# Kernel optimization log

Measured on AMD Instinct MI355X. Metric: run time of the kernel, lower is better.

The kernel has to match this reference:

```python
import jax, jax.numpy as jnp
import numpy as np

H = 4          # num attention heads
C1 = 64        # channel_num[0]
C2 = 128       # channel_num[1]
KV = C1 + C2   # 192
MLP = C1 * 4   # expand_ratio=4


def _layernorm(x, g, b, eps=1e-6):
    m = jnp.mean(x, axis=-1, keepdims=True)
    v = jnp.mean((x - m) ** 2, axis=-1, keepdims=True)
    return (x - m) * jax.lax.rsqrt(v + eps) * g + b


def setup_inputs() -> dict:
    key = jax.random.key(0)
    ks = jax.random.split(key, 12)
    B, N = 8, 3136
    s_q = 1.0 / np.sqrt(C1)
    s_kv = 1.0 / np.sqrt(KV)
    return {
        "emb1": jax.random.normal(ks[0], (B, N, C1), jnp.float32),
        "emb2": jax.random.normal(ks[1], (B, N, C2), jnp.float32),
        # per-head projection weights (nn.Linear convention: y = x @ W.T)
        "Wq": jax.random.uniform(ks[2], (H, C1, C1), jnp.float32, -s_q, s_q),
        "Wk": jax.random.uniform(ks[3], (H, KV, KV), jnp.float32, -s_kv, s_kv),
        "Wv": jax.random.uniform(ks[4], (H, KV, KV), jnp.float32, -s_kv, s_kv),
        "Wout": jax.random.uniform(ks[5], (C1, C1), jnp.float32, -s_q, s_q),
        "ln1_g": jnp.ones((C1,), jnp.float32),
        "ln1_b": jnp.zeros((C1,), jnp.float32),
        "lnall_g": jnp.ones((KV,), jnp.float32),
        "lnall_b": jnp.zeros((KV,), jnp.float32),
        "ffn_g": jnp.ones((C1,), jnp.float32),
        "ffn_b": jnp.zeros((C1,), jnp.float32),
        "fc1_w": jax.random.uniform(ks[6], (MLP, C1), jnp.float32, -s_q, s_q),
        "fc1_b": jnp.zeros((MLP,), jnp.float32),
        "fc2_w": jax.random.uniform(ks[7], (C1, MLP), jnp.float32, -1.0 / np.sqrt(MLP), 1.0 / np.sqrt(MLP)),
        "fc2_b": jnp.zeros((C1,), jnp.float32),
    }


def reference(emb1, emb2, Wq, Wk, Wv, Wout, ln1_g, ln1_b, lnall_g, lnall_b,
              ffn_g, ffn_b, fc1_w, fc1_b, fc2_w, fc2_b):
    # emb1: [B,N,C1], emb2: [B,N,C2]
    emb_all = jnp.concatenate([emb1, emb2], axis=2)          # [B,N,KV]
    cx1 = _layernorm(emb1, ln1_g, ln1_b)                     # [B,N,C1]
    ea = _layernorm(emb_all, lnall_g, lnall_b)               # [B,N,KV]

    # batched per-head projections (replaces Python loop over ModuleList)
    qT = jnp.einsum('bnc,hdc->bhdn', cx1, Wq)                # [B,H,C1,N]
    k = jnp.einsum('bnk,hdk->bhnd', ea, Wk)                  # [B,H,N,KV]
    vT = jnp.einsum('bnk,hdk->bhdn', ea, Wv)                 # [B,H,KV,N]

    scores = jnp.einsum('bhcn,bhnk->bhck', qT, k) / np.sqrt(KV)  # [B,H,C1,KV]
    # InstanceNorm2d over spatial dims (C1, KV) per (batch, head), affine=False
    m = jnp.mean(scores, axis=(2, 3), keepdims=True)
    v = jnp.mean((scores - m) ** 2, axis=(2, 3), keepdims=True)
    scores = (scores - m) * jax.lax.rsqrt(v + 1e-5)
    probs = jax.nn.softmax(scores, axis=3)                   # softmax over KV

    ctx = jnp.einsum('bhck,bhkn->bhcn', probs, vT)           # [B,H,C1,N]
    ctx = jnp.mean(ctx, axis=1).transpose(0, 2, 1)           # mean over heads -> [B,N,C1]
    o = ctx @ Wout.T                                         # [B,N,C1]

    cx = emb1 + o                                            # residual
    x = _layernorm(cx, ffn_g, ffn_b)
    x = jax.nn.gelu(x @ fc1_w.T + fc1_b, approximate=False)
    x = x @ fc2_w.T + fc2_b
    return x + cx
```

## Files before the change

### kernel.cpp

```cpp
#include <hip/hip_runtime.h>
#include <hip/hip_bf16.h>

typedef __hip_bfloat16 bf;
typedef unsigned short ushort_t;
typedef __attribute__((ext_vector_type(8))) short short8;
typedef __attribute__((ext_vector_type(4))) float f32x4;

#define NB 8
#define SEQ 3136
#define HD 4

__device__ __forceinline__ float lo_bf(unsigned u){ return __uint_as_float(u << 16); }
__device__ __forceinline__ float hi_bf(unsigned u){ return __uint_as_float(u & 0xffff0000u); }
__device__ __forceinline__ float b16f(ushort_t s){ return __uint_as_float(((unsigned)s) << 16); }
__device__ __forceinline__ unsigned short f2bfbits(float f){
  unsigned u = __float_as_uint(f);
  unsigned r = u + 0x7fffu + ((u >> 16) & 1u);
  return (unsigned short)(r >> 16);
}
__device__ __forceinline__ float ldin(const void* p, long i, bool isbf){
  return isbf ? __bfloat162float(((const bf*)p)[i]) : ((const float*)p)[i];
}
__device__ __forceinline__ float4 ld4(const void* p, long i, bool isbf){
  if (isbf){
    uint2 u = *reinterpret_cast<const uint2*>((const unsigned short*)p + i);
    return make_float4(lo_bf(u.x), hi_bf(u.x), lo_bf(u.y), hi_bf(u.y));
  }
  const float* f = (const float*)p + i;
  return make_float4(f[0], f[1], f[2], f[3]);
}
__device__ __forceinline__ short8 ldfrag(const void* p, long i, bool isbf){
  if (isbf) return *reinterpret_cast<const short8*>((const unsigned short*)p + i);
  const float* f = (const float*)p + i;
  short8 r;
  #pragma unroll
  for (int q=0;q<8;++q) r[q] = (short)f2bfbits(f[q]);
  return r;
}
#define DTYPE_FLAG(p) (((const unsigned*)(p))[0] == 0x3F803F80u)

__device__ __forceinline__ float wsum(float v){
  #pragma unroll
  for (int o = 32; o > 0; o >>= 1) v += __shfl_xor(v, o, 64);
  return v;
}
__device__ __forceinline__ float wmax(float v){
  #pragma unroll
  for (int o = 32; o > 0; o >>= 1) v = fmaxf(v, __shfl_xor(v, o, 64));
  return v;
}

__global__ __launch_bounds__(256) void k_g(
    const void* __restrict__ emb1, const void* __restrict__ emb2,
    const void* __restrict__ g1, const void* __restrict__ b1,
    const void* __restrict__ ga, const void* __restrict__ ba,
    ushort_t* __restrict__ part, ushort_t* __restrict__ eag){
  bool isbf = DTYPE_FLAG(g1);
  __shared__ __align__(16) ushort_t z1t[64*72];
  __shared__ __align__(16) ushort_t zat[192*72];
  int tid = threadIdx.x, wave = tid >> 6, lane = tid & 63;
  int quad = lane >> 4, nl = lane & 15;
  int b = blockIdx.y, ch = blockIdx.x;
  long t0 = (long)b*SEQ + ch*64;
  float g1l = ldin(g1,lane,isbf), b1l = ldin(b1,lane,isbf);
  float ga0 = ldin(ga,lane,isbf),     ba0 = ldin(ba,lane,isbf);
  float ga1 = ldin(ga,64+lane,isbf),  ba1 = ldin(ba,64+lane,isbf);
  float ga2 = ldin(ga,128+lane,isbf), ba2 = ldin(ba,128+lane,isbf);
  #pragma unroll 4
  for (int k = 0; k < 16; ++k){
    int tok = wave*16 + k;
    long t = t0 + tok;
    float e1  = ldin(emb1, t*64 + lane, isbf);
    float e2a = ldin(emb2, t*128 + lane, isbf);
    float e2b = ldin(emb2, t*128 + 64 + lane, isbf);
    float s1 = wsum(e1), ss1 = wsum(e1*e1);
    float m1 = s1*(1.f/64.f);
    float r1 = rsqrtf(fmaxf(ss1*(1.f/64.f) - m1*m1, 0.f) + 1e-6f);
    z1t[lane*72 + tok] = f2bfbits((e1 - m1)*r1*g1l + b1l);
    float s23 = wsum(e2a+e2b), ss23 = wsum(e2a*e2a + e2b*e2b);
    float ma = (s1+s23)*(1.f/192.f);
    float ra = rsqrtf(fmaxf((ss1+ss23)*(1.f/192.f) - ma*ma, 0.f) + 1e-6f);
    unsigned short za0 = f2bfbits((e1  - ma)*ra*ga0 + ba0);
    unsigned short za1 = f2bfbits((e2a - ma)*ra*ga1 + ba1);
    unsigned short za2 = f2bfbits((e2b - ma)*ra*ga2 + ba2);
    zat[lane*72 + tok]       = za0;
    zat[(64+lane)*72 + tok]  = za1;
    zat[(128+lane)*72 + tok] = za2;
    eag[t*192 + lane]       = za0;
    eag[t*192 + 64 + lane]  = za1;
    eag[t*192 + 128 + lane] = za2;
  }
  __syncthreads();
  short8 a0 = *reinterpret_cast<const short8*>(&z1t[(wave*16+nl)*72 + quad*8]);
  short8 a1 = *reinterpret_cast<const short8*>(&z1t[(wave*16+nl)*72 + 32 + quad*8]);
  ushort_t* P = part + ((long)b*49 + ch)*12288;
  #pragma unroll
  for (int nt = 0; nt < 12; ++nt){
    f32x4 cd = {0.f,0.f,0.f,0.f};
    short8 b0 = *reinterpret_cast<const short8*>(&zat[(nt*16+nl)*72 + quad*8]);
    cd = __builtin_amdgcn_mfma_f32_16x16x32_bf16(a0, b0, cd, 0, 0, 0);
    short8 b1v = *reinterpret_cast<const short8*>(&zat[(nt*16+nl)*72 + 32 + quad*8]);
    cd = __builtin_amdgcn_mfma_f32_16x16x32_bf16(a1, b1v, cd, 0, 0, 0);
    #pragma unroll
    for (int reg = 0; reg < 4; ++reg)
      P[(wave*16 + quad*4 + reg)*192 + nt*16 + nl] = f2bfbits(cd[reg]);
  }
}

__global__ __launch_bounds__(64) void k_red(
    const ushort_t* __restrict__ part, float* __restrict__ G){
  int idx4 = blockIdx.x*64 + threadIdx.x;
  int b = idx4 / 3072, e4 = idx4 - b*3072;
  const ushort_t* p = part + (long)b*49*12288 + e4*4;
  float s0=0.f, s1=0.f, s2=0.f, s3=0.f;
  #pragma unroll
  for (int ch = 0; ch < 49; ++ch){
    uint2 u = *reinterpret_cast<const uint2*>(p + (long)ch*12288);
    s0 += lo_bf(u.x); s1 += hi_bf(u.x); s2 += lo_bf(u.y); s3 += hi_bf(u.y);
  }
  ((float4*)G)[idx4] = make_float4(s0,s1,s2,s3);
}

__global__ __launch_bounds__(256) void k_s(
    const float* __restrict__ G, const void* __restrict__ Wq, const void* __restrict__ Wk,
    const void* __restrict__ lng, float* __restrict__ S){
  bool isbf = DTYPE_FLAG(lng);
  __shared__ __align__(16) ushort_t sGb[64*200];
  __shared__ __align__(16) ushort_t sT[48*72];
  int ec = blockIdx.x, h = blockIdx.y, b = blockIdx.z;
  int e0 = ec*48;
  int tid = threadIdx.x, wave = tid >> 6, lane = tid & 63;
  int quad = lane >> 4, nl = lane & 15;
  const float4* Gb4 = (const float4*)(G + (long)b*12288);
  for (int i16 = tid; i16 < 3072; i16 += 256){
    float4 v = Gb4[i16];
    int e = i16*4; int c = e/192, j = e - c*192;
    unsigned lo = (unsigned)f2bfbits(v.x) | ((unsigned)f2bfbits(v.y) << 16);
    unsigned hi = (unsigned)f2bfbits(v.z) | ((unsigned)f2bfbits(v.w) << 16);
    *reinterpret_cast<uint2*>(&sGb[c*200 + j]) = make_uint2(lo, hi);
  }
  __syncthreads();
  long wk0 = (long)h*36864;
  short8 aG[6];
  #pragma unroll
  for (int ks = 0; ks < 6; ++ks)
    aG[ks] = *reinterpret_cast<const short8*>(&sGb[(wave*16+nl)*200 + ks*32 + quad*8]);
  #pragma unroll
  for (int nt = 0; nt < 3; ++nt){
    f32x4 cd = {0.f,0.f,0.f,0.f};
    #pragma unroll
    for (int ks = 0; ks < 6; ++ks){
      short8 bw = ldfrag(Wk, wk0 + (long)(e0 + nt*16+nl)*192 + ks*32 + quad*8, isbf);
      cd = __builtin_amdgcn_mfma_f32_16x16x32_bf16(aG[ks], bw, cd, 0, 0, 0);
    }
    #pragma unroll
    for (int reg = 0; reg < 4; ++reg)
      sT[(nt*16+nl)*72 + wave*16 + quad*4 + reg] = f2bfbits(cd[reg]);
  }
  __syncthreads();
  long wq0 = (long)h*4096;
  short8 aQ[2];
  #pragma unroll
  for (int ks = 0; ks < 2; ++ks)
    aQ[ks] = ldfrag(Wq, wq0 + (long)(wave*16+nl)*64 + ks*32 + quad*8, isbf);
  const float scale = 0.07216878364870323f;
  float* Sb = S + ((long)b*HD + h)*12288;
  #pragma unroll
  for (int nt = 0; nt < 3; ++nt){
    f32x4 cd = {0.f,0.f,0.f,0.f};
    #pragma unroll
    for (int ks = 0; ks < 2; ++ks){
      short8 bt = *reinterpret_cast<const short8*>(&sT[(nt*16+nl)*72 + ks*32 + quad*8]);
      cd = __builtin_amdgcn_mfma_f32_16x16x32_bf16(aQ[ks], bt, cd, 0, 0, 0);
    }
    #pragma unroll
    for (int reg = 0; reg < 4; ++reg)
      Sb[(wave*16 + quad*4 + reg)*192 + e0 + nt*16 + nl] = cd[reg]*scale;
  }
}

__global__ __launch_bounds__(256) void k_smpv(
    const float* __restrict__ S, const void* __restrict__ Wv,
    const void* __restrict__ lng, float* __restrict__ Mh){
  bool isbf = DTYPE_FLAG(lng);
  __shared__ __align__(16) float sP[64*196];
  __shared__ __align__(16) unsigned sWv[192*52];
  __shared__ float red[8];
  __shared__ float stat[2];
  int jc = blockIdx.x, h = blockIdx.y, b = blockIdx.z;
  const float* Sb = S + ((long)b*HD + h)*12288;
  int tid = threadIdx.x, wave = tid >> 6, lane = tid & 63;
  long wv0 = (long)h*36864;
  float ps = 0.f, pss = 0.f;
  const float4* Sb4 = (const float4*)Sb;
  for (int i16 = tid; i16 < 3072; i16 += 256){
    float4 v = Sb4[i16];
    int e = i16*4; int c = e/192, j = e - c*192;
    *reinterpret_cast<float4*>(&sP[c*196 + j]) = v;
    ps += v.x + v.y + v.z + v.w;
    pss += v.x*v.x + v.y*v.y + v.z*v.z + v.w*v.w;
  }
  if (isbf){
    const unsigned short* wvp = (const unsigned short*)Wv + wv0 + jc*96;
    for (int idx = tid; idx < 4608; idx += 256){
      int r = idx/24, c2 = idx - r*24;
      uint2 v = *reinterpret_cast<const uint2*>(wvp + (long)r*192 + c2*4);
      *reinterpret_cast<uint2*>(&sWv[r*52 + c2*2]) = v;
    }
  } else {
    for (int idx = tid; idx < 9216; idx += 256){
      int r = idx/48, c = idx - r*48;
      float a0 = ldin(Wv, wv0 + (long)r*192 + jc*96 + c*2,     false);
      float a1 = ldin(Wv, wv0 + (long)r*192 + jc*96 + c*2 + 1, false);
      sWv[r*52 + c] = (unsigned)f2bfbits(a0) | ((unsigned)f2bfbits(a1) << 16);
    }
  }
  ps = wsum(ps); pss = wsum(pss);
  if (lane == 0){ red[wave] = ps; red[4+wave] = pss; }
  __syncthreads();
  if (tid == 0){
    float s  = red[0]+red[1]+red[2]+red[3];
    float s2 = red[4]+red[5]+red[6]+red[7];
    float m = s * (1.f/12288.f);
    stat[0] = m;
    stat[1] = rsqrtf(fmaxf(s2*(1.f/12288.f) - m*m, 0.f) + 1e-5f);
  }
  __syncthreads();
  float m = stat[0], r = stat[1];
  for (int rr = 0; rr < 16; ++rr){
    int row = wave*16 + rr;
    float v0 = (sP[row*196+lane]     - m)*r;
    float v1 = (sP[row*196+64+lane]  - m)*r;
    float v2 = (sP[row*196+128+lane] - m)*r;
    float mx = wmax(fmaxf(v0, fmaxf(v1, v2)));
    float e0 = __expf(v0-mx), e1 = __expf(v1-mx), e2 = __expf(v2-mx);
    float inv = 1.f / wsum(e0+e1+e2);
    sP[row*196+lane]     = e0*inv;
    sP[row*196+64+lane]  = e1*inv;
    sP[row*196+128+lane] = e2*inv;
  }
  __syncthreads();
  int ty = tid >> 4, tx = tid & 15;
  int j0 = jc*96 + tx*6;
  float acc[4][6];
  #pragma unroll
  for (int i=0;i<4;++i) for (int q=0;q<6;++q) acc[i][q]=0.f;
  #pragma unroll 2
  for (int e = 0; e < 192; ++e){
    float p4[4];
    #pragma unroll
    for (int i=0;i<4;++i) p4[i] = sP[(ty*4+i)*196 + e];
    unsigned wa = sWv[e*52 + tx*3];
    unsigned wb = sWv[e*52 + tx*3 + 1];
    unsigned wc = sWv[e*52 + tx*3 + 2];
    float w0 = lo_bf(wa), w1 = hi_bf(wa), w2 = lo_bf(wb),
          w3 = hi_bf(wb), w4 = lo_bf(wc), w5 = hi_bf(wc);
    #pragma unroll
    for (int i=0;i<4;++i){
      acc[i][0] = fmaf(p4[i], w0, acc[i][0]);
      acc[i][1] = fmaf(p4[i], w1, acc[i][1]);
      acc[i][2] = fmaf(p4[i], w2, acc[i][2]);
      acc[i][3] = fmaf(p4[i], w3, acc[i][3]);
      acc[i][4] = fmaf(p4[i], w4, acc[i][4]);
      acc[i][5] = fmaf(p4[i], w5, acc[i][5]);
    }
  }
  float* Mb = Mh + ((long)b*HD + h)*12288;
  #pragma unroll
  for (int i=0;i<4;++i)
    #pragma unroll
    for (int q=0;q<6;++q)
      Mb[(ty*4+i)*192 + j0 + q] = acc[i][q];
}

__global__ __launch_bounds__(256) void k_w2(
    const float* __restrict__ Mh, const void* __restrict__ Wout,
    const void* __restrict__ lng, ushort_t* __restrict__ W2){
  bool isbf = DTYPE_FLAG(lng);
  __shared__ __align__(16) float sM[64*49];
  int jc = blockIdx.x, b = blockIdx.y;
  int tid = threadIdx.x;
  for (int idx = tid; idx < 3072; idx += 256){
    int c = idx/48, j = idx - c*48;
    long base = (long)b*HD*12288 + c*192 + jc*48 + j;
    float s = Mh[base] + Mh[base+12288] + Mh[base+2*12288] + Mh[base+3*12288];
    sM[c*49 + j] = 0.25f*s;
  }
  __syncthreads();
  int ty = tid >> 4, tx = tid & 15;
  float acc[4][3];
  #pragma unroll
  for (int i=0;i<4;++i) for (int q=0;q<3;++q) acc[i][q]=0.f;
  for (int c = 0; c < 64; c += 4){
    float4 w4[4];
    #pragma unroll
    for (int i=0;i<4;++i) w4[i] = ld4(Wout, (long)(ty*4+i)*64 + c, isbf);
    float ww[4][4];
    #pragma unroll
    for (int i=0;i<4;++i){ ww[i][0]=w4[i].x; ww[i][1]=w4[i].y; ww[i][2]=w4[i].z; ww[i][3]=w4[i].w; }
    #pragma unroll
    for (int u = 0; u < 4; ++u){
      float t3[3];
      #pragma unroll
      for (int q=0;q<3;++q) t3[q] = sM[(c+u)*49 + tx*3 + q];
      #pragma unroll
      for (int i=0;i<4;++i)
        #pragma unroll
        for (int q=0;q<3;++q) acc[i][q] = fmaf(ww[i][u], t3[q], acc[i][q]);
    }
  }
  ushort_t* W2b = W2 + (long)b*12288;
  #pragma unroll
  for (int i=0;i<4;++i)
    #pragma unroll
    for (int q=0;q<3;++q)
      W2b[(ty*4+i)*192 + jc*48 + tx*3 + q] = f2bfbits(acc[i][q]);
}

__global__ __launch_bounds__(256) void k_tail(
    const void* __restrict__ emb1, const ushort_t* __restrict__ eag,
    const ushort_t* __restrict__ W2g,
    const void* __restrict__ ffg, const void* __restrict__ ffb,
    const void* __restrict__ f1w, const void* __restrict__ f1b,
    const void* __restrict__ f2w, const void* __restrict__ f2b,
    const void* __restrict__ lng, void* __restrict__ out){
  bool isbf = DTYPE_FLAG(lng);
  __shared__ __align__(16) ushort_t sCX[16*72];
  __shared__ __align__(16) ushort_t sX[16*88];
  __shared__ __align__(16) ushort_t sH[16*280];
  int tid = threadIdx.x, wave = tid >> 6, lane = tid & 63;
  int quad = lane >> 4, nl = lane & 15;
  int b = blockIdx.y;
  long tbase = (long)b*SEQ + blockIdx.x*16;

  short8 aO[6];
  #pragma unroll
  for (int kt = 0; kt < 6; ++kt)
    aO[kt] = *reinterpret_cast<const short8*>(eag + (tbase + nl)*192 + kt*32 + quad*8);
  const ushort_t* W2b = W2g + (long)b*12288;
  {
    f32x4 cd = {0.f,0.f,0.f,0.f};
    #pragma unroll
    for (int kt = 0; kt < 6; ++kt){
      short8 bf8 = *reinterpret_cast<const short8*>(W2b + (wave*16+nl)*192 + kt*32 + quad*8);
      cd = __builtin_amdgcn_mfma_f32_16x16x32_bf16(aO[kt], bf8, cd, 0, 0, 0);
    }
    #pragma unroll
    for (int reg = 0; reg < 4; ++reg){
      int tokl = quad*4 + reg;
      int chn = wave*16 + nl;
      float e1v = ldin(emb1, (tbase + tokl)*64 + chn, isbf);
      sCX[tokl*72 + chn] = f2bfbits(cd[reg] + e1v);
    }
  }
  __syncthreads();

  float gl = ldin(ffg, lane, isbf), bl = ldin(ffb, lane, isbf);
  #pragma unroll
  for (int k = 0; k < 4; ++k){
    int tokl = wave*4 + k;
    float c = b16f(sCX[tokl*72 + lane]);
    float s = wsum(c), ss = wsum(c*c);
    float m = s*(1.f/64.f);
    float r = rsqrtf(fmaxf(ss*(1.f/64.f) - m*m, 0.f) + 1e-6f);
    sX[tokl*88 + lane] = f2bfbits((c - m)*r*gl + bl);
  }
  __syncthreads();

  short8 aX[2];
  #pragma unroll
  for (int kt = 0; kt < 2; ++kt)
    aX[kt] = *reinterpret_cast<const short8*>(&sX[nl*88 + kt*32 + quad*8]);
  #pragma unroll
  for (int nn = 0; nn < 4; ++nn){
    int nt = wave*4 + nn;
    f32x4 cd = {0.f,0.f,0.f,0.f};
    #pragma unroll
    for (int kt = 0; kt < 2; ++kt){
      short8 bf8 = ldfrag(f1w, (long)(nt*16+nl)*64 + kt*32 + quad*8, isbf);
      cd = __builtin_amdgcn_mfma_f32_16x16x32_bf16(aX[kt], bf8, cd, 0, 0, 0);
    }
    float bb = ldin(f1b, nt*16+nl, isbf);
    #pragma unroll
    for (int reg = 0; reg < 4; ++reg){
      float v = cd[reg] + bb;
      float h = 0.5f*v*(1.f + erff(v*0.70710678118654752f));
      sH[(quad*4 + reg)*280 + nt*16 + nl] = f2bfbits(h);
    }
  }
  __syncthreads();

  short8 aH[8];
  #pragma unroll
  for (int kt = 0; kt < 8; ++kt)
    aH[kt] = *reinterpret_cast<const short8*>(&sH[nl*280 + kt*32 + quad*8]);
  {
    f32x4 cd = {0.f,0.f,0.f,0.f};
    #pragma unroll
    for (int kt = 0; kt < 8; ++kt){
      short8 bf8 = ldfrag(f2w, (long)(wave*16+nl)*256 + kt*32 + quad*8, isbf);
      cd = __builtin_amdgcn_mfma_f32_16x16x32_bf16(aH[kt], bf8, cd, 0, 0, 0);
    }
    float bb2 = ldin(f2b, wave*16+nl, isbf);
    #pragma unroll
    for (int reg = 0; reg < 4; ++reg){
      int tokl = quad*4 + reg;
      int chn = wave*16 + nl;
      float y = cd[reg] + bb2 + b16f(sCX[tokl*72 + chn]);
      if (isbf) sCX[tokl*72 + chn] = f2bfbits(y);
      else ((float*)out)[(tbase + tokl)*64 + chn] = y;
    }
  }
  if (isbf){
    __syncthreads();
    int tokl = wave*4 + (lane >> 4), prt = lane & 15;
    uint2 v = *reinterpret_cast<const uint2*>(&sCX[tokl*72 + prt*4]);
    *reinterpret_cast<uint2*>((ushort_t*)out + (tbase + tokl)*64 + prt*4) = v;
  }
}

extern "C" void kernel_launch(void* const* d_in, const int* in_sizes, int n_in,
                              void* d_out, int out_size, void* d_ws, size_t ws_size,
                              hipStream_t stream){
  const void* emb1 = d_in[0];
  const void* emb2 = d_in[1];
  const void* Wq   = d_in[2];
  const void* Wk   = d_in[3];
  const void* Wv   = d_in[4];
  const void* Wout = d_in[5];
  const void* ln1g = d_in[6];
  const void* ln1b = d_in[7];
  const void* lag  = d_in[8];
  const void* lab  = d_in[9];
  const void* ffg  = d_in[10];
  const void* ffb  = d_in[11];
  const void* f1w  = d_in[12];
  const void* f1b  = d_in[13];
  const void* f2w  = d_in[14];
  const void* f2b  = d_in[15];

  char* base = (char*)d_ws;
  ushort_t* part = (ushort_t*)base;
  ushort_t* ea   = (ushort_t*)(base + 9633792);
  float*    G    = (float*)(base + 19267584);
  float*    S    = (float*)(base + 19660800);
  float*    Mh   = (float*)(base + 21233664);
  ushort_t* W2   = (ushort_t*)(base + 22806528);

  k_g   <<<dim3(49,NB),   256, 0, stream>>>(emb1, emb2, ln1g, ln1b, lag, lab, part, ea);
  k_red <<<384,            64, 0, stream>>>(part, G);
  k_s   <<<dim3(4,HD,NB), 256, 0, stream>>>(G, Wq, Wk, ln1g, S);
  k_smpv<<<dim3(2,HD,NB), 256, 0, stream>>>(S, Wv, ln1g, Mh);
  k_w2  <<<dim3(4,NB),    256, 0, stream>>>(Mh, Wout, ln1g, W2);
  k_tail<<<dim3(196,NB),  256, 0, stream>>>(emb1, ea, W2, ffg, ffb,
                                            f1w, f1b, f2w, f2b, ln1g, d_out);
}
```

Before: 204.5 us.

## Batch loads in LayerNorm/Gram kernel and split softmax-V kernel into more blocks

k_g now issues loads for four tokens before doing their reductions, so more global-memory requests are in flight at once. k_smpv is split into four column chunks of 48 instead of two of 96, which doubles the grid from 64 to 128 blocks and stores Wv in shared memory as 16-bit values. Each block repeats the instance-norm and softmax work, so that part is now done twice as often. A tanh-based gelu helper is added but is not called by any code shown.

```diff
diff --git a/kernel.cpp b/kernel.cpp
--- a/kernel.cpp
+++ b/kernel.cpp
@@ -48,6 +48,10 @@
   #pragma unroll
   for (int o = 32; o > 0; o >>= 1) v = fmaxf(v, __shfl_xor(v, o, 64));
   return v;
+}
+__device__ __forceinline__ float gelu_f(float v){
+  float u = v*(0.7978845608f + 0.0356774081f*v*v);
+  return v * __builtin_amdgcn_rcpf(1.f + __expf(-2.f*u));
 }
 
 __global__ __launch_bounds__(256) void k_g(
@@ -66,29 +70,37 @@
   float ga0 = ldin(ga,lane,isbf),     ba0 = ldin(ba,lane,isbf);
   float ga1 = ldin(ga,64+lane,isbf),  ba1 = ldin(ba,64+lane,isbf);
   float ga2 = ldin(ga,128+lane,isbf), ba2 = ldin(ba,128+lane,isbf);
-  #pragma unroll 4
-  for (int k = 0; k < 16; ++k){
-    int tok = wave*16 + k;
-    long t = t0 + tok;
-    float e1  = ldin(emb1, t*64 + lane, isbf);
-    float e2a = ldin(emb2, t*128 + lane, isbf);
-    float e2b = ldin(emb2, t*128 + 64 + lane, isbf);
-    float s1 = wsum(e1), ss1 = wsum(e1*e1);
-    float m1 = s1*(1.f/64.f);
-    float r1 = rsqrtf(fmaxf(ss1*(1.f/64.f) - m1*m1, 0.f) + 1e-6f);
-    z1t[lane*72 + tok] = f2bfbits((e1 - m1)*r1*g1l + b1l);
-    float s23 = wsum(e2a+e2b), ss23 = wsum(e2a*e2a + e2b*e2b);
-    float ma = (s1+s23)*(1.f/192.f);
-    float ra = rsqrtf(fmaxf((ss1+ss23)*(1.f/192.f) - ma*ma, 0.f) + 1e-6f);
-    unsigned short za0 = f2bfbits((e1  - ma)*ra*ga0 + ba0);
-    unsigned short za1 = f2bfbits((e2a - ma)*ra*ga1 + ba1);
-    unsigned short za2 = f2bfbits((e2b - ma)*ra*ga2 + ba2);
-    zat[lane*72 + tok]       = za0;
-    zat[(64+lane)*72 + tok]  = za1;
-    zat[(128+lane)*72 + tok] = za2;
-    eag[t*192 + lane]       = za0;
-    eag[t*192 + 64 + lane]  = za1;
-    eag[t*192 + 128 + lane] = za2;
+  #pragma unroll
+  for (int k4 = 0; k4 < 4; ++k4){
+    float e1[4], e2a[4], e2b[4];
+    #pragma unroll
+    for (int u = 0; u < 4; ++u){
+      long t = t0 + wave*16 + k4 + u*4;
+      e1[u]  = ldin(emb1, t*64 + lane, isbf);
+      e2a[u] = ldin(emb2, t*128 + lane, isbf);
+      e2b[u] = ldin(emb2, t*128 + 64 + lane, isbf);
+    }
+    #pragma unroll
+    for (int u = 0; u < 4; ++u){
+      int tok = wave*16 + k4 + u*4;
+      long t = t0 + tok;
+      float s1 = wsum(e1[u]), ss1 = wsum(e1[u]*e1[u]);
+      float m1 = s1*(1.f/64.f);
+      float r1 = rsqrtf(fmaxf(ss1*(1.f/64.f) - m1*m1, 0.f) + 1e-6f);
+      z1t[lane*72 + tok] = f2bfbits((e1[u] - m1)*r1*g1l + b1l);
+      float s23 = wsum(e2a[u]+e2b[u]), ss23 = wsum(e2a[u]*e2a[u] + e2b[u]*e2b[u]);
+      float ma = (s1+s23)*(1.f/192.f);
+      float ra = rsqrtf(fmaxf((ss1+ss23)*(1.f/192.f) - ma*ma, 0.f) + 1e-6f);
+      unsigned short za0 = f2bfbits((e1[u]  - ma)*ra*ga0 + ba0);
+      unsigned short za1 = f2bfbits((e2a[u] - ma)*ra*ga1 + ba1);
+      unsigned short za2 = f2bfbits((e2b[u] - ma)*ra*ga2 + ba2);
+      zat[lane*72 + tok]       = za0;
+      zat[(64+lane)*72 + tok]  = za1;
+      zat[(128+lane)*72 + tok] = za2;
+      eag[t*192 + lane]       = za0;
+      eag[t*192 + 64 + lane]  = za1;
+      eag[t*192 + 128 + lane] = za2;
+    }
   }
   __syncthreads();
   short8 a0 = *reinterpret_cast<const short8*>(&z1t[(wave*16+nl)*72 + quad*8]);
@@ -184,7 +196,7 @@
     const void* __restrict__ lng, float* __restrict__ Mh){
   bool isbf = DTYPE_FLAG(lng);
   __shared__ __align__(16) float sP[64*196];
-  __shared__ __align__(16) unsigned sWv[192*52];
+  __shared__ __align__(16) ushort_t sWv[192*52];
   __shared__ float red[8];
   __shared__ float stat[2];
   int jc = blockIdx.x, h = blockIdx.y, b = blockIdx.z;
@@ -201,18 +213,16 @@
     pss += v.x*v.x + v.y*v.y + v.z*v.z + v.w*v.w;
   }
   if (isbf){
-    const unsigned short* wvp = (const unsigned short*)Wv + wv0 + jc*96;
-    for (int idx = tid; idx < 4608; idx += 256){
-      int r = idx/24, c2 = idx - r*24;
+    const ushort_t* wvp = (const ushort_t*)Wv + wv0 + jc*48;
+    for (int idx = tid; idx < 2304; idx += 256){
+      int r = idx/12, c2 = idx - r*12;
       uint2 v = *reinterpret_cast<const uint2*>(wvp + (long)r*192 + c2*4);
-      *reinterpret_cast<uint2*>(&sWv[r*52 + c2*2]) = v;
+      *reinterpret_cast<uint2*>(&sWv[r*52 + c2*4]) = v;
     }
   } else {
     for (int idx = tid; idx < 9216; idx += 256){
       int r = idx/48, c = idx - r*48;
-      float a0 = ldin(Wv, wv0 + (long)r*192 + jc*96 + c*2,     false);
-      float a1 = ldin(Wv, wv0 + (long)r*192 + jc*96 + c*2 + 1, false);
-      sWv[r*52 + c] = (unsigned)f2bfbits(a0) | ((unsigned)f2bfbits(a1) << 16);
+      sWv[r*52 + c] = f2bfbits(ldin(Wv, wv0 + (long)r*192 + jc*48 + c, false));
     }
   }
   ps = wsum(ps); pss = wsum(pss);
@@ -241,35 +251,30 @@
   }
   __syncthreads();
   int ty = tid >> 4, tx = tid & 15;
-  int j0 = jc*96 + tx*6;
-  float acc[4][6];
-  #pragma unroll
-  for (int i=0;i<4;++i) for (int q=0;q<6;++q) acc[i][q]=0.f;
-  #pragma unroll 2
+  int j0 = jc*48 + tx*3;
+  float acc[4][3];
+  #pragma unroll
+  for (int i=0;i<4;++i) for (int q=0;q<3;++q) acc[i][q]=0.f;
+  #pragma unroll 4
   for (int e = 0; e < 192; ++e){
     float p4[4];
     #pragma unroll
     for (int i=0;i<4;++i) p4[i] = sP[(ty*4+i)*196 + e];
-    unsigned wa = sWv[e*52 + tx*3];
-    unsigned wb = sWv[e*52 + tx*3 + 1];
-    unsigned wc = sWv[e*52 + tx*3 + 2];
-    float w0 = lo_bf(wa), w1 = hi_bf(wa), w2 = lo_bf(wb),
-          w3 = hi_bf(wb), w4 = lo_bf(wc), w5 = hi_bf(wc);
+    float w0 = b16f(sWv[e*52 + tx*3]);
+    float w1 = b16f(sWv[e*52 + tx*3 + 1]);
+    float w2 = b16f(sWv[e*52 + tx*3 + 2]);
     #pragma unroll
     for (int i=0;i<4;++i){
       acc[i][0] = fmaf(p4[i], w0, acc[i][0]);
       acc[i][1] = fmaf(p4[i], w1, acc[i][1]);
       acc[i][2] = fmaf(p4[i], w2, acc[i][2]);
-      acc[i][3] = fmaf(p4[i], w3, acc[i][3]);
-      acc[i][4] = fmaf(p4[i], w4, acc[i][4]);
-      acc[i][5] = fmaf(p4[i], w5, acc[i][5]);
     }
   }
   float* Mb = Mh + ((long)b*HD + h)*12288;
   #pragma unroll
   for (int i=0;i<4;++i)
     #pragma unroll
-    for (int q=0;q<6;++q)
+    for (int q=0;q<3;++q)
       Mb[(ty*4+i)*192 + j0 + q] = acc[i][q];
 }
 
@@ -450,7 +455,7 @@
   k_g   <<<dim3(49,NB),   256, 0, stream>>>(emb1, emb2, ln1g, ln1b, lag, lab, part, ea);
   k_red <<<384,            64, 0, stream>>>(part, G);
   k_s   <<<dim3(4,HD,NB), 256, 0, stream>>>(G, Wq, Wk, ln1g, S);
-  k_smpv<<<dim3(2,HD,NB), 256, 0, stream>>>(S, Wv, ln1g, Mh);
+  k_smpv<<<dim3(4,HD,NB), 256, 0, stream>>>(S, Wv, ln1g, Mh);
   k_w2  <<<dim3(4,NB),    256, 0, stream>>>(Mh, Wout, ln1g, W2);
   k_tail<<<dim3(196,NB),  256, 0, stream>>>(emb1, ea, W2, ffg, ffb,
                                             f1w, f1b, f2w, f2b, ln1g, d_out);
```

Result: slower. 217.6 us (+6.4%).

## Move instance-norm stats into k_s and split k_smpv across more blocks

Applied to the files above, without the earlier changes.

k_s now reduces per-block partial sums and sums of squares of the scores and writes them to a small stat buffer. k_smpv reads those partials instead of scanning the whole score matrix itself. That lets k_smpv split rows into 4 chunks and columns into 4 chunks, giving 512 blocks instead of 64, with each thread computing 3 outputs. The intent is to fill more CUs in this small stage and drop the redundant full-matrix load and block reduction. In exchange, each block does less arithmetic per load and there is an extra global stat buffer.

```diff
diff --git a/kernel.cpp b/kernel.cpp
--- a/kernel.cpp
+++ b/kernel.cpp
@@ -123,10 +123,11 @@
 
 __global__ __launch_bounds__(256) void k_s(
     const float* __restrict__ G, const void* __restrict__ Wq, const void* __restrict__ Wk,
-    const void* __restrict__ lng, float* __restrict__ S){
+    const void* __restrict__ lng, float* __restrict__ S, float* __restrict__ pstat){
   bool isbf = DTYPE_FLAG(lng);
   __shared__ __align__(16) ushort_t sGb[64*200];
   __shared__ __align__(16) ushort_t sT[48*72];
+  __shared__ float red[8];
   int ec = blockIdx.x, h = blockIdx.y, b = blockIdx.z;
   int e0 = ec*48;
   int tid = threadIdx.x, wave = tid >> 6, lane = tid & 63;
@@ -165,6 +166,7 @@
     aQ[ks] = ldfrag(Wq, wq0 + (long)(wave*16+nl)*64 + ks*32 + quad*8, isbf);
   const float scale = 0.07216878364870323f;
   float* Sb = S + ((long)b*HD + h)*12288;
+  float ps = 0.f, pss = 0.f;
   #pragma unroll
   for (int nt = 0; nt < 3; ++nt){
     f32x4 cd = {0.f,0.f,0.f,0.f};
@@ -174,103 +176,90 @@
       cd = __builtin_amdgcn_mfma_f32_16x16x32_bf16(aQ[ks], bt, cd, 0, 0, 0);
     }
     #pragma unroll
-    for (int reg = 0; reg < 4; ++reg)
-      Sb[(wave*16 + quad*4 + reg)*192 + e0 + nt*16 + nl] = cd[reg]*scale;
+    for (int reg = 0; reg < 4; ++reg){
+      float v = cd[reg]*scale;
+      Sb[(wave*16 + quad*4 + reg)*192 + e0 + nt*16 + nl] = v;
+      ps += v; pss += v*v;
+    }
+  }
+  ps = wsum(ps); pss = wsum(pss);
+  if (lane == 0){ red[wave] = ps; red[4+wave] = pss; }
+  __syncthreads();
+  if (tid == 0){
+    float s  = red[0]+red[1]+red[2]+red[3];
+    float s2 = red[4]+red[5]+red[6]+red[7];
+    float* st = pstat + ((long)b*HD + h)*8 + ec*2;
+    st[0] = s; st[1] = s2;
   }
 }
 
 __global__ __launch_bounds__(256) void k_smpv(
     const float* __restrict__ S, const void* __restrict__ Wv,
+    const float* __restrict__ pstat,
     const void* __restrict__ lng, float* __restrict__ Mh){
   bool isbf = DTYPE_FLAG(lng);
-  __shared__ __align__(16) float sP[64*196];
-  __shared__ __align__(16) unsigned sWv[192*52];
-  __shared__ float red[8];
-  __shared__ float stat[2];
-  int jc = blockIdx.x, h = blockIdx.y, b = blockIdx.z;
-  const float* Sb = S + ((long)b*HD + h)*12288;
+  __shared__ __align__(16) float sS[16*196];
+  __shared__ __align__(16) ushort_t sWv[192*52];
+  int jc = blockIdx.x, rc = blockIdx.y, hb = blockIdx.z;
+  int h = hb & 3, b = hb >> 2;
   int tid = threadIdx.x, wave = tid >> 6, lane = tid & 63;
   long wv0 = (long)h*36864;
-  float ps = 0.f, pss = 0.f;
-  const float4* Sb4 = (const float4*)Sb;
-  for (int i16 = tid; i16 < 3072; i16 += 256){
+  const float* st = pstat + (long)hb*8;
+  float s  = st[0] + st[2] + st[4] + st[6];
+  float s2 = st[1] + st[3] + st[5] + st[7];
+  float m = s * (1.f/12288.f);
+  float rv = rsqrtf(fmaxf(s2*(1.f/12288.f) - m*m, 0.f) + 1e-5f);
+  const float4* Sb4 = (const float4*)(S + ((long)hb)*12288 + rc*16*192);
+  for (int i16 = tid; i16 < 768; i16 += 256){
     float4 v = Sb4[i16];
-    int e = i16*4; int c = e/192, j = e - c*192;
-    *reinterpret_cast<float4*>(&sP[c*196 + j]) = v;
-    ps += v.x + v.y + v.z + v.w;
-    pss += v.x*v.x + v.y*v.y + v.z*v.z + v.w*v.w;
+    int e = i16*4; int r = e/192, j = e - r*192;
+    *reinterpret_cast<float4*>(&sS[r*196 + j]) = v;
   }
   if (isbf){
-    const unsigned short* wvp = (const unsigned short*)Wv + wv0 + jc*96;
-    for (int idx = tid; idx < 4608; idx += 256){
-      int r = idx/24, c2 = idx - r*24;
+    const ushort_t* wvp = (const ushort_t*)Wv + wv0 + jc*48;
+    for (int idx = tid; idx < 2304; idx += 256){
+      int r = idx/12, c2 = idx - r*12;
       uint2 v = *reinterpret_cast<const uint2*>(wvp + (long)r*192 + c2*4);
-      *reinterpret_cast<uint2*>(&sWv[r*52 + c2*2]) = v;
+      *reinterpret_cast<uint2*>(&sWv[r*52 + c2*4]) = v;
     }
   } else {
     for (int idx = tid; idx < 9216; idx += 256){
       int r = idx/48, c = idx - r*48;
-      float a0 = ldin(Wv, wv0 + (long)r*192 + jc*96 + c*2,     false);
-      float a1 = ldin(Wv, wv0 + (long)r*192 + jc*96 + c*2 + 1, false);
-      sWv[r*52 + c] = (unsigned)f2bfbits(a0) | ((unsigned)f2bfbits(a1) << 16);
-    }
-  }
-  ps = wsum(ps); pss = wsum(pss);
-  if (lane == 0){ red[wave] = ps; red[4+wave] = pss; }
-  __syncthreads();
-  if (tid == 0){
-    float s  = red[0]+red[1]+red[2]+red[3];
-    float s2 = red[4]+red[5]+red[6]+red[7];
-    float m = s * (1.f/12288.f);
-    stat[0] = m;
-    stat[1] = rsqrtf(fmaxf(s2*(1.f/12288.f) - m*m, 0.f) + 1e-5f);
-  }
-  __syncthreads();
-  float m = stat[0], r = stat[1];
-  for (int rr = 0; rr < 16; ++rr){
-    int row = wave*16 + rr;
-    float v0 = (sP[row*196+lane]     - m)*r;
-    float v1 = (sP[row*196+64+lane]  - m)*r;
-    float v2 = (sP[row*196+128+lane] - m)*r;
+      sWv[r*52 + c] = f2bfbits(ldin(Wv, wv0 + (long)r*192 + jc*48 + c, false));
+    }
+  }
+  __syncthreads();
+  #pragma unroll
+  for (int k = 0; k < 4; ++k){
+    int row = wave*4 + k;
+    float v0 = (sS[row*196+lane]     - m)*rv;
+    float v1 = (sS[row*196+64+lane]  - m)*rv;
+    float v2 = (sS[row*196+128+lane] - m)*rv;
     float mx = wmax(fmaxf(v0, fmaxf(v1, v2)));
     float e0 = __expf(v0-mx), e1 = __expf(v1-mx), e2 = __expf(v2-mx);
     float inv = 1.f / wsum(e0+e1+e2);
-    sP[row*196+lane]     = e0*inv;
-    sP[row*196+64+lane]  = e1*inv;
-    sP[row*196+128+lane] = e2*inv;
-  }
-  __syncthreads();
-  int ty = tid >> 4, tx = tid & 15;
-  int j0 = jc*96 + tx*6;
-  float acc[4][6];
-  #pragma unroll
-  for (int i=0;i<4;++i) for (int q=0;q<6;++q) acc[i][q]=0.f;
-  #pragma unroll 2
+    sS[row*196+lane]     = e0*inv;
+    sS[row*196+64+lane]  = e1*inv;
+    sS[row*196+128+lane] = e2*inv;
+  }
+  __syncthreads();
+  int row = tid >> 4, tx = tid & 15;
+  float acc0 = 0.f, acc1 = 0.f, acc2 = 0.f;
+  #pragma unroll 8
   for (int e = 0; e < 192; ++e){
-    float p4[4];
-    #pragma unroll
-    for (int i=0;i<4;++i) p4[i] = sP[(ty*4+i)*196 + e];
-    unsigned wa = sWv[e*52 + tx*3];
-    unsigned wb = sWv[e*52 + tx*3 + 1];
-    unsigned wc = sWv[e*52 + tx*3 + 2];
-    float w0 = lo_bf(wa), w1 = hi_bf(wa), w2 = lo_bf(wb),
-          w3 = hi_bf(wb), w4 = lo_bf(wc), w5 = hi_bf(wc);
-    #pragma unroll
-    for (int i=0;i<4;++i){
-      acc[i][0] = fmaf(p4[i], w0, acc[i][0]);
-      acc[i][1] = fmaf(p4[i], w1, acc[i][1]);
-      acc[i][2] = fmaf(p4[i], w2, acc[i][2]);
-      acc[i][3] = fmaf(p4[i], w3, acc[i][3]);
-      acc[i][4] = fmaf(p4[i], w4, acc[i][4]);
-      acc[i][5] = fmaf(p4[i], w5, acc[i][5]);
-    }
-  }
-  float* Mb = Mh + ((long)b*HD + h)*12288;
-  #pragma unroll
-  for (int i=0;i<4;++i)
-    #pragma unroll
-    for (int q=0;q<6;++q)
-      Mb[(ty*4+i)*192 + j0 + q] = acc[i][q];
+    float p = sS[row*196 + e];
+    float w0 = b16f(sWv[e*52 + tx*3]);
+    float w1 = b16f(sWv[e*52 + tx*3 + 1]);
+    float w2 = b16f(sWv[e*52 + tx*3 + 2]);
+    acc0 = fmaf(p, w0, acc0);
+    acc1 = fmaf(p, w1, acc1);
+    acc2 = fmaf(p, w2, acc2);
+  }
+  float* Mb = Mh + (long)hb*12288;
+  int j0 = jc*48 + tx*3;
+  Mb[(rc*16 + row)*192 + j0]     = acc0;
+  Mb[(rc*16 + row)*192 + j0 + 1] = acc1;
+  Mb[(rc*16 + row)*192 + j0 + 2] = acc2;
 }
 
 __global__ __launch_bounds__(256) void k_w2(
@@ -446,12 +435,13 @@
   float*    S    = (float*)(base + 19660800);
   float*    Mh   = (float*)(base + 21233664);
   ushort_t* W2   = (ushort_t*)(base + 22806528);
-
-  k_g   <<<dim3(49,NB),   256, 0, stream>>>(emb1, emb2, ln1g, ln1b, lag, lab, part, ea);
-  k_red <<<384,            64, 0, stream>>>(part, G);
-  k_s   <<<dim3(4,HD,NB), 256, 0, stream>>>(G, Wq, Wk, ln1g, S);
-  k_smpv<<<dim3(2,HD,NB), 256, 0, stream>>>(S, Wv, ln1g, Mh);
-  k_w2  <<<dim3(4,NB),    256, 0, stream>>>(Mh, Wout, ln1g, W2);
-  k_tail<<<dim3(196,NB),  256, 0, stream>>>(emb1, ea, W2, ffg, ffb,
-                                            f1w, f1b, f2w, f2b, ln1g, d_out);
-}
+  float*    pstat= (float*)(base + 23003136);
+
+  k_g   <<<dim3(49,NB),     256, 0, stream>>>(emb1, emb2, ln1g, ln1b, lag, lab, part, ea);
+  k_red <<<384,              64, 0, stream>>>(part, G);
+  k_s   <<<dim3(4,HD,NB),   256, 0, stream>>>(G, Wq, Wk, ln1g, S, pstat);
+  k_smpv<<<dim3(4,4,NB*HD), 256, 0, stream>>>(S, Wv, pstat, ln1g, Mh);
+  k_w2  <<<dim3(4,NB),      256, 0, stream>>>(Mh, Wout, ln1g, W2);
+  k_tail<<<dim3(196,NB),    256, 0, stream>>>(emb1, ea, W2, ffg, ffb,
+                                              f1w, f1b, f2w, f2b, ln1g, d_out);
+}
```

New measurement: 229.9 us. +12.4%, slower.
